# Kernel tuning notes

Hardware: AMD Instinct MI355X
Metric: run time of the kernel (lower is better)

## Reference

```python
import jax, jax.numpy as jnp
import numpy as np

N = 50000
E = 800000
IN_C = 128
HID = 128
HID2 = 256
OUT_C = 40


def setup_inputs() -> dict:
    key = jax.random.key(0)
    ks = jax.random.split(key, 12)
    x = jax.random.normal(ks[0], (N, IN_C), dtype=jnp.float32)
    edge_index = jax.random.randint(ks[1], (2, E), 0, N, dtype=jnp.int64)
    def lin(k, fi, fo):
        # torch Linear default init: U(-1/sqrt(fi), 1/sqrt(fi))
        b = 1.0 / np.sqrt(fi)
        k1, k2 = jax.random.split(k)
        W = jax.random.uniform(k1, (fi, fo), minval=-b, maxval=b, dtype=jnp.float32)
        bvec = jax.random.uniform(k2, (fo,), minval=-b, maxval=b, dtype=jnp.float32)
        return W, bvec
    W1, b1 = lin(ks[2], IN_C, HID)
    W2, b2 = lin(ks[3], HID, HID)
    W3, b3 = lin(ks[4], HID, HID2)
    W4, b4 = lin(ks[5], HID2, HID2)
    Wl, bl = lin(ks[6], HID2, OUT_C)
    return {"x": x, "edge_index": edge_index,
            "W1": W1, "b1": b1, "W2": W2, "b2": b2,
            "W3": W3, "b3": b3, "W4": W4, "b4": b4,
            "Wl": Wl, "bl": bl}


def gin_conv(x, src, dst, Wa, ba, Wb, bb):
    # GINConv, eps=0: h_i = MLP(x_i + sum_{j->i} x_j)
    agg = jax.ops.segment_sum(x[src], dst, num_segments=N)  # [N, d]
    h = x + agg
    h = jax.nn.relu(h @ Wa + ba)
    return h @ Wb + bb


def reference(x, edge_index, W1, b1, W2, b2, W3, b3, W4, b4, Wl, bl):
    src, dst = edge_index[0], edge_index[1]
    h = jax.nn.relu(gin_conv(x, src, dst, W1, b1, W2, b2))
    # dropout p=0.5 is identity in eval mode
    h = jax.nn.relu(gin_conv(h, src, dst, W3, b3, W4, b4))
    return h @ Wl + bl
```

## Files before the change

kernel.cpp:

```cpp
#include <hip/hip_runtime.h>
#include <hip/hip_bf16.h>
#include <hip/hip_fp16.h>
#include <stdint.h>

#define N_NODES 50000
#define E_EDGES 800000
#define NBKT 196
#define PBUF 6144

typedef short s16x8 __attribute__((ext_vector_type(8)));
typedef _Float16 f16x8 __attribute__((ext_vector_type(8)));
typedef float f32x4 __attribute__((ext_vector_type(4)));

__device__ __forceinline__ unsigned short f2h_bits(float f) {
    return __half_as_ushort(__float2half(f));
}
__device__ __forceinline__ float h2f(unsigned short u) {
    __half h = *reinterpret_cast<const __half*>(&u);
    return __half2float(h);
}
__device__ __forceinline__ float2 h2f2(unsigned int u) {
    __half2 h = *reinterpret_cast<const __half2*>(&u);
    return __half22float2(h);
}

__global__ __launch_bounds__(256) void khist_conv(
    const int* __restrict__ dst, int* __restrict__ gbcnt,
    const float* __restrict__ x, unsigned short* __restrict__ xh) {
    __shared__ int bcnt[NBKT];
    int t = threadIdx.x;
    for (int i = t; i < NBKT; i += 256) bcnt[i] = 0;
    __syncthreads();
    int gid = blockIdx.x * 256 + t;
    const int STRIDE = 256 * 256;
    const float4* xv = (const float4*)x;
    for (int e = gid; e < E_EDGES; e += STRIDE) {
        atomicAdd(&bcnt[dst[e] >> 8], 1);
        float4 a = xv[(size_t)2 * e];
        float4 b = xv[(size_t)2 * e + 1];
        s16x8 h;
        h[0] = (short)f2h_bits(a.x); h[1] = (short)f2h_bits(a.y);
        h[2] = (short)f2h_bits(a.z); h[3] = (short)f2h_bits(a.w);
        h[4] = (short)f2h_bits(b.x); h[5] = (short)f2h_bits(b.y);
        h[6] = (short)f2h_bits(b.z); h[7] = (short)f2h_bits(b.w);
        *(s16x8*)(xh + (size_t)e * 8) = h;
    }
    __syncthreads();
    for (int i = t; i < NBKT; i += 256) atomicAdd(&gbcnt[i], bcnt[i]);
}

__global__ void scan_bkt(const int* __restrict__ gbcnt, int* __restrict__ bscan,
                         int* __restrict__ gcur) {
    __shared__ int wsum[4];
    int t = threadIdx.x, lane = t & 63, wid = t >> 6;
    int v = (t < NBKT) ? gbcnt[t] : 0;
    int x = v;
#pragma unroll
    for (int off = 1; off < 64; off <<= 1) {
        int tt = __shfl_up(x, off);
        if (lane >= off) x += tt;
    }
    if (lane == 63) wsum[wid] = x;
    __syncthreads();
    if (t == 0) {
        int s = 0;
#pragma unroll
        for (int i = 0; i < 4; i++) { int tmp = wsum[i]; wsum[i] = s; s += tmp; }
    }
    __syncthreads();
    int excl = x - v + wsum[wid];
    if (t <= NBKT) bscan[t] = excl;
    if (t < NBKT) gcur[t] = excl;
}

__global__ __launch_bounds__(256) void bin_pass(
    const int* __restrict__ src, const int* __restrict__ dst,
    int* __restrict__ gcur, unsigned int* __restrict__ pool) {
    __shared__ unsigned int lbuf[NBKT][64];
    __shared__ int lcnt[NBKT];
    __shared__ int lbase[NBKT];
    int tid = threadIdx.x;
    for (int i = tid; i < NBKT; i += 256) lcnt[i] = 0;
    __syncthreads();
    const int EPG = (E_EDGES + gridDim.x - 1) / gridDim.x;
    int e0 = blockIdx.x * EPG;
    int e1 = e0 + EPG; if (e1 > E_EDGES) e1 = E_EDGES;
    for (int wbase = e0; wbase < e1; wbase += 2048) {
        int wend = wbase + 2048; if (wend > e1) wend = e1;
        int d8[8], s8[8], n8 = 0;
        {
            int e = wbase + tid;
#pragma unroll
            for (int k = 0; k < 8; k++, e += 256)
                if (e < wend) { d8[n8] = dst[e]; s8[n8] = src[e]; n8++; }
        }
        for (int k = 0; k < n8; k++) {
            int d = d8[k];
            unsigned int rec = (unsigned int)(s8[k] & 0xFFFF) |
                               ((unsigned int)(d & 255) << 16);
            int b = d >> 8;
            int slot = atomicAdd(&lcnt[b], 1);
            if (slot < 64) lbuf[b][slot] = rec;
            else pool[atomicAdd(&gcur[b], 1)] = rec;
        }
        __syncthreads();
        if (tid < NBKT) {
            int c = lcnt[tid]; if (c > 64) c = 64;
            int lines = c >> 5;
            if (lines) lbase[tid] = atomicAdd(&gcur[tid], lines * 32);
        }
        __syncthreads();
        {
            int wid = tid >> 6, lane = tid & 63;
            for (int b = wid * 49; b < (wid + 1) * 49; b++) {
                int c = lcnt[b]; if (c > 64) c = 64;
                int lines = c >> 5, rem = c & 31;
                for (int l = 0; l < lines; l++)
                    if (lane < 32)
                        pool[lbase[b] + l * 32 + lane] = lbuf[b][l * 32 + lane];
                if (lines && lane < rem) lbuf[b][lane] = lbuf[b][lines * 32 + lane];
                if (lane == 0) lcnt[b] = rem;
            }
        }
        __syncthreads();
    }
    if (tid < NBKT) {
        int c = lcnt[tid]; if (c > 64) c = 64;
        if (c) lbase[tid] = atomicAdd(&gcur[tid], c);
    }
    __syncthreads();
    {
        int wid = tid >> 6, lane = tid & 63;
        for (int b = wid * 49; b < (wid + 1) * 49; b++) {
            int c = lcnt[b]; if (c > 64) c = 64;
            if (lane < c) pool[lbase[b] + lane] = lbuf[b][lane];
        }
    }
}

__global__ __launch_bounds__(256) void build_csr(
    const unsigned int* __restrict__ pool, const int* __restrict__ bscan,
    int* __restrict__ rowptr, unsigned short* __restrict__ perm) {
    __shared__ int ncnt[256];
    __shared__ int ncur[256];
    __shared__ int wsum[4];
    __shared__ unsigned short pbuf[PBUF];
    int b = blockIdx.x, t = threadIdx.x;
    int base = bscan[b], K = bscan[b + 1] - base;
    ncnt[t] = 0;
    __syncthreads();
    for (int i = t; i < K; i += 256)
        atomicAdd(&ncnt[(pool[base + i] >> 16) & 255], 1);
    __syncthreads();
    int lane = t & 63, wid = t >> 6;
    int v = ncnt[t], x = v;
#pragma unroll
    for (int off = 1; off < 64; off <<= 1) {
        int tt = __shfl_up(x, off);
        if (lane >= off) x += tt;
    }
    if (lane == 63) wsum[wid] = x;
    __syncthreads();
    if (t == 0) {
        int s = 0;
#pragma unroll
        for (int i = 0; i < 4; i++) { int tmp = wsum[i]; wsum[i] = s; s += tmp; }
    }
    __syncthreads();
    int excl = x - v + wsum[wid];
    int node = b * 256 + t;
    if (node <= N_NODES) rowptr[node] = base + excl;
    ncur[t] = excl;
    __syncthreads();
    for (int i = t; i < K; i += 256) {
        unsigned int rec = pool[base + i];
        int nl = (rec >> 16) & 255;
        int pos = atomicAdd(&ncur[nl], 1);
        if (pos < PBUF) pbuf[pos] = (unsigned short)rec;
        else perm[base + pos] = (unsigned short)rec;
    }
    __syncthreads();
    int KK = K < PBUF ? K : PBUF;
    for (int i = t; i < KK; i += 256) perm[base + i] = pbuf[i];
}

__global__ __launch_bounds__(256) void gather_agg_h(
    const unsigned short* __restrict__ feat,
    const int* __restrict__ rowptr,
    const unsigned short* __restrict__ perm,
    unsigned short* __restrict__ out) {
    int node = (blockIdx.x * 256 + threadIdx.x) >> 6;
    if (node >= N_NODES) return;
    int lane = threadIdx.x & 63;
    const unsigned int* fv = (const unsigned int*)feat;
    float2 acc = h2f2(fv[(size_t)node * 64 + lane]);
    int beg = rowptr[node], end = rowptr[node + 1];
    for (int base = beg; base < end; base += 64) {
        int cnt = end - base; if (cnt > 64) cnt = 64;
        int pv = (base + lane < end) ? (int)perm[base + lane] : 0;
        int j = 0;
        for (; j + 3 < cnt; j += 4) {
            int s0 = __shfl(pv, j);
            int s1 = __shfl(pv, j + 1);
            int s2 = __shfl(pv, j + 2);
            int s3 = __shfl(pv, j + 3);
            unsigned int u0 = fv[(size_t)s0 * 64 + lane];
            unsigned int u1 = fv[(size_t)s1 * 64 + lane];
            unsigned int u2 = fv[(size_t)s2 * 64 + lane];
            unsigned int u3 = fv[(size_t)s3 * 64 + lane];
            float2 f0 = h2f2(u0), f1 = h2f2(u1), f2 = h2f2(u2), f3 = h2f2(u3);
            acc.x += (f0.x + f1.x) + (f2.x + f3.x);
            acc.y += (f0.y + f1.y) + (f2.y + f3.y);
        }
        for (; j < cnt; j++) {
            int s = __shfl(pv, j);
            float2 f = h2f2(fv[(size_t)s * 64 + lane]);
            acc.x += f.x;
            acc.y += f.y;
        }
    }
    unsigned int o = (unsigned int)f2h_bits(acc.x) | ((unsigned int)f2h_bits(acc.y) << 16);
    ((unsigned int*)out)[(size_t)node * 64 + lane] = o;
}

__device__ __forceinline__ void prep_one(const float* __restrict__ W,
                                         unsigned short* __restrict__ Whi,
                                         unsigned short* __restrict__ Wlo,
                                         int K, int F, int Fpad, int i) {
    int S = K / 32, T = Fpad / 16;
    int total = T * S * 64;
    if (i >= total) return;
    int lane = i & 63;
    int s = (i >> 6) % S;
    int t = (i >> 6) / S;
    int col = t * 16 + (lane & 15);
    int k0 = s * 32 + (lane >> 4) * 8;
    s16x8 vh, vl;
#pragma unroll
    for (int j = 0; j < 8; j++) {
        float w = (col < F) ? W[(size_t)(k0 + j) * F + col] : 0.f;
        unsigned short h = f2h_bits(w);
        float r = (w - h2f(h)) * 1024.0f;
        vh[j] = (short)h;
        vl[j] = (short)f2h_bits(r);
    }
    *(s16x8*)(Whi + (size_t)i * 8) = vh;
    *(s16x8*)(Wlo + (size_t)i * 8) = vl;
}

__global__ void prep_all(const float* W1, const float* W2, const float* W3,
                         const float* W4, const float* Wl,
                         unsigned short* W1h, unsigned short* W1l,
                         unsigned short* W2h, unsigned short* W2l,
                         unsigned short* W3h, unsigned short* W3l,
                         unsigned short* W4h, unsigned short* W4l,
                         unsigned short* Wlh, unsigned short* Wll) {
    int b = blockIdx.x, t = threadIdx.x;
    if (b < 8)       prep_one(W1, W1h, W1l, 128, 128, 128, b * 256 + t);
    else if (b < 16) prep_one(W2, W2h, W2l, 128, 128, 128, (b - 8) * 256 + t);
    else if (b < 32) prep_one(W3, W3h, W3l, 128, 256, 256, (b - 16) * 256 + t);
    else if (b < 64) prep_one(W4, W4h, W4l, 256, 256, 256, (b - 32) * 256 + t);
    else             prep_one(Wl, Wlh, Wll, 256, 40, 64, (b - 64) * 256 + t);
}

template <int K, int F, int FOUT, bool RELU, int RPW, bool HOUT>
__global__ __launch_bounds__(256) void gemm_h(
    const unsigned short* __restrict__ A,
    const unsigned short* __restrict__ Whi,
    const unsigned short* __restrict__ Wlo,
    const float* __restrict__ bias,
    float* __restrict__ out) {
    constexpr int S = K / 32;
    constexpr int T = F / 16;
    constexpr int TL = T / 4;
    int wave = threadIdx.x >> 6;
    int lane = threadIdx.x & 63;
    int row0 = blockIdx.x * (16 * RPW);
    if (row0 >= N_NODES) return;
    int lm = lane & 15;
    int quad = lane >> 4;
    bool rv[RPW];
#pragma unroll
    for (int r = 0; r < RPW; r++) rv[r] = (row0 + r * 16) < N_NODES;

    f16x8 a[RPW][S];
#pragma unroll
    for (int r = 0; r < RPW; r++) {
        int rr = rv[r] ? row0 + r * 16 : row0;
        const unsigned short* ap = A + (size_t)(rr + lm) * K + quad * 8;
#pragma unroll
        for (int s = 0; s < S; s++)
            a[r][s] = *(const f16x8*)(ap + s * 32);
    }

    f32x4 accH[TL][RPW], accL[TL][RPW];
#pragma unroll
    for (int t = 0; t < TL; t++)
#pragma unroll
        for (int r = 0; r < RPW; r++) {
            f32x4 z = {0.f, 0.f, 0.f, 0.f};
            accH[t][r] = z;
            accL[t][r] = z;
        }

#pragma unroll
    for (int s = 0; s < S; s++) {
#pragma unroll
        for (int t = 0; t < TL; t++) {
            int tg = wave * TL + t;
            const size_t fi = (size_t)((tg * S + s) * 64 + lane) * 8;
            const f16x8 bh = *(const f16x8*)(Whi + fi);
            const f16x8 bl = *(const f16x8*)(Wlo + fi);
#pragma unroll
            for (int r = 0; r < RPW; r++) {
                accH[t][r] = __builtin_amdgcn_mfma_f32_16x16x32_f16(a[r][s], bh, accH[t][r], 0, 0, 0);
                accL[t][r] = __builtin_amdgcn_mfma_f32_16x16x32_f16(a[r][s], bl, accL[t][r], 0, 0, 0);
            }
        }
    }

    const float ls = 1.0f / 1024.0f;
#pragma unroll
    for (int r = 0; r < RPW; r++) {
        if (!rv[r]) break;
        int orow = row0 + r * 16 + quad * 4;
#pragma unroll
        for (int t = 0; t < TL; t++) {
            int col = (wave * TL + t) * 16 + lm;
            if (FOUT < F && col >= FOUT) continue;
            float bv = bias[col];
#pragma unroll
            for (int q = 0; q < 4; q++) {
                float vv = fmaf(accL[t][r][q], ls, accH[t][r][q]) + bv;
                if (RELU) vv = fmaxf(vv, 0.f);
                if (HOUT) {
                    ((unsigned short*)out)[(size_t)(orow + q) * FOUT + col] = f2h_bits(vv);
                } else {
                    out[(size_t)(orow + q) * FOUT + col] = vv;
                }
            }
        }
    }
}

extern "C" void kernel_launch(void* const* d_in, const int* in_sizes, int n_in,
                              void* d_out, int out_size, void* d_ws, size_t ws_size,
                              hipStream_t stream) {
    const float* x  = (const float*)d_in[0];
    const int* ei   = (const int*)d_in[1];
    const float* W1 = (const float*)d_in[2];
    const float* b1 = (const float*)d_in[3];
    const float* W2 = (const float*)d_in[4];
    const float* b2 = (const float*)d_in[5];
    const float* W3 = (const float*)d_in[6];
    const float* b3 = (const float*)d_in[7];
    const float* W4 = (const float*)d_in[8];
    const float* b4 = (const float*)d_in[9];
    const float* Wl = (const float*)d_in[10];
    const float* bl = (const float*)d_in[11];
    float* out = (float*)d_out;

    const int* src = ei;
    const int* dst = ei + E_EDGES;

    char* ws = (char*)d_ws;
    size_t off = 0;
    unsigned short* xh  = (unsigned short*)(ws + off); off += (size_t)N_NODES * 128 * 2;
    unsigned short* hFh = (unsigned short*)(ws + off); off += (size_t)N_NODES * 128 * 2;
    unsigned short* h1h = (unsigned short*)(ws + off); off += (size_t)N_NODES * 128 * 2;
    unsigned short* h2h = (unsigned short*)(ws + off); off += (size_t)N_NODES * 256 * 2;
    unsigned short* h2bh= (unsigned short*)(ws + off); off += (size_t)N_NODES * 256 * 2;
    unsigned short* W1h = (unsigned short*)(ws + off); off += 16384 * 2;
    unsigned short* W1l = (unsigned short*)(ws + off); off += 16384 * 2;
    unsigned short* W2h = (unsigned short*)(ws + off); off += 16384 * 2;
    unsigned short* W2l = (unsigned short*)(ws + off); off += 16384 * 2;
    unsigned short* W3h = (unsigned short*)(ws + off); off += 32768 * 2;
    unsigned short* W3l = (unsigned short*)(ws + off); off += 32768 * 2;
    unsigned short* W4h = (unsigned short*)(ws + off); off += 65536 * 2;
    unsigned short* W4l = (unsigned short*)(ws + off); off += 65536 * 2;
    unsigned short* Wlh = (unsigned short*)(ws + off); off += 16384 * 2;
    unsigned short* Wll = (unsigned short*)(ws + off); off += 16384 * 2;
    off = (off + 255) & ~(size_t)255;
    unsigned int* pool = (unsigned int*)(ws + off); off += (size_t)E_EDGES * 4;
    unsigned short* perm = (unsigned short*)(ws + off); off += (size_t)E_EDGES * 2;
    off = (off + 255) & ~(size_t)255;
    int* rowptr = (int*)(ws + off); off += (size_t)(N_NODES + 1) * 4;
    int* gbcnt  = (int*)(ws + off); off += 256 * 4;
    int* bscan  = (int*)(ws + off); off += 256 * 4;
    int* gcur   = (int*)(ws + off); off += 256 * 4;
    (void)ws_size; (void)in_sizes; (void)n_in; (void)out_size;

    (void)hipMemsetAsync(gbcnt, 0, 256 * 4, stream);
    khist_conv<<<256, 256, 0, stream>>>(dst, gbcnt, x, xh);
    scan_bkt<<<1, 256, 0, stream>>>(gbcnt, bscan, gcur);
    bin_pass<<<256, 256, 0, stream>>>(src, dst, gcur, pool);
    build_csr<<<NBKT, 256, 0, stream>>>(pool, bscan, rowptr, perm);

    prep_all<<<72, 256, 0, stream>>>(W1, W2, W3, W4, Wl,
                                     W1h, W1l, W2h, W2l, W3h, W3l,
                                     W4h, W4l, Wlh, Wll);

    const int aggBlocks = (N_NODES * 64 + 255) / 256;
    const int rblk = (N_NODES + 31) / 32;

    gather_agg_h<<<aggBlocks, 256, 0, stream>>>(xh, rowptr, perm, hFh);
    gemm_h<128, 128, 128, true, 2, true><<<rblk, 256, 0, stream>>>(hFh, W1h, W1l, b1, (float*)h1h);
    gemm_h<128, 128, 128, true, 2, true><<<rblk, 256, 0, stream>>>(h1h, W2h, W2l, b2, (float*)xh);

    gather_agg_h<<<aggBlocks, 256, 0, stream>>>(xh, rowptr, perm, hFh);
    gemm_h<128, 256, 256, true, 2, true><<<rblk, 256, 0, stream>>>(hFh, W3h, W3l, b3, (float*)h2h);
    gemm_h<256, 256, 256, true, 2, true><<<rblk, 256, 0, stream>>>(h2h, W4h, W4l, b4, (float*)h2bh);

    gemm_h<256, 64, 40, false, 2, false><<<rblk, 256, 0, stream>>>(h2bh, Wlh, Wll, bl, out);
}
```

Measured before the change: 315.1 us.

## Store fp16 features in column-panel layout and gather per panel

Feature matrices are now stored as 32-column fp16 panels (panel-major, node-minor) instead of row-major, and the gather kernel processes one 64-byte panel slice per node, with four 16-lane groups handling four neighbors at once and a shuffle reduction at the end. The GEMM loads and half-precision stores are adapted to the panel layout. The aim is to shrink each panel's working set so random neighbor gathers hit in cache better, at the cost of four times as many gather blocks, more passes over rowptr/perm, and 64-byte rather than 256-byte gather granularity. Only the 128-wide layers use the gather; the 256-wide GEMM outputs use the same panel indexing.

```diff
diff --git a/kernel.cpp b/kernel.cpp
--- a/kernel.cpp
+++ b/kernel.cpp
@@ -23,6 +23,7 @@
     __half2 h = *reinterpret_cast<const __half2*>(&u);
     return __half22float2(h);
 }
+
 
 __global__ __launch_bounds__(256) void khist_conv(
     const int* __restrict__ dst, int* __restrict__ gbcnt,
@@ -43,7 +44,8 @@
         h[2] = (short)f2h_bits(a.z); h[3] = (short)f2h_bits(a.w);
         h[4] = (short)f2h_bits(b.x); h[5] = (short)f2h_bits(b.y);
         h[6] = (short)f2h_bits(b.z); h[7] = (short)f2h_bits(b.w);
-        *(s16x8*)(xh + (size_t)e * 8) = h;
+        int nodei = e >> 4, col8 = e & 15;
+        *(s16x8*)(xh + ((size_t)(col8 >> 2) * N_NODES + nodei) * 32 + (col8 & 3) * 8) = h;
     }
     __syncthreads();
     for (int i = t; i < NBKT; i += 256) atomicAdd(&gbcnt[i], bcnt[i]);
@@ -184,43 +186,41 @@
     for (int i = t; i < KK; i += 256) perm[base + i] = pbuf[i];
 }
 
-__global__ __launch_bounds__(256) void gather_agg_h(
+__global__ __launch_bounds__(256) void gather_pass(
     const unsigned short* __restrict__ feat,
     const int* __restrict__ rowptr,
     const unsigned short* __restrict__ perm,
     unsigned short* __restrict__ out) {
-    int node = (blockIdx.x * 256 + threadIdx.x) >> 6;
-    if (node >= N_NODES) return;
+    const int BPP = N_NODES / 4;
+    int p = blockIdx.x / BPP;
+    int node = (blockIdx.x % BPP) * 4 + (threadIdx.x >> 6);
     int lane = threadIdx.x & 63;
-    const unsigned int* fv = (const unsigned int*)feat;
-    float2 acc = h2f2(fv[(size_t)node * 64 + lane]);
+    int grp = lane >> 4, c = lane & 15;
+    const unsigned int* pl = (const unsigned int*)feat + (size_t)p * N_NODES * 16;
+    unsigned int* po = (unsigned int*)out + (size_t)p * N_NODES * 16;
+    float2 acc = {0.f, 0.f};
+    if (grp == 0) acc = h2f2(pl[(size_t)node * 16 + c]);
     int beg = rowptr[node], end = rowptr[node + 1];
     for (int base = beg; base < end; base += 64) {
-        int cnt = end - base; if (cnt > 64) cnt = 64;
+        int wlen = end - base; if (wlen > 64) wlen = 64;
         int pv = (base + lane < end) ? (int)perm[base + lane] : 0;
-        int j = 0;
-        for (; j + 3 < cnt; j += 4) {
-            int s0 = __shfl(pv, j);
-            int s1 = __shfl(pv, j + 1);
-            int s2 = __shfl(pv, j + 2);
-            int s3 = __shfl(pv, j + 3);
-            unsigned int u0 = fv[(size_t)s0 * 64 + lane];
-            unsigned int u1 = fv[(size_t)s1 * 64 + lane];
-            unsigned int u2 = fv[(size_t)s2 * 64 + lane];
-            unsigned int u3 = fv[(size_t)s3 * 64 + lane];
-            float2 f0 = h2f2(u0), f1 = h2f2(u1), f2 = h2f2(u2), f3 = h2f2(u3);
-            acc.x += (f0.x + f1.x) + (f2.x + f3.x);
-            acc.y += (f0.y + f1.y) + (f2.y + f3.y);
-        }
-        for (; j < cnt; j++) {
-            int s = __shfl(pv, j);
-            float2 f = h2f2(fv[(size_t)s * 64 + lane]);
-            acc.x += f.x;
-            acc.y += f.y;
-        }
-    }
-    unsigned int o = (unsigned int)f2h_bits(acc.x) | ((unsigned int)f2h_bits(acc.y) << 16);
-    ((unsigned int*)out)[(size_t)node * 64 + lane] = o;
+        for (int j = 0; j < wlen; j += 4) {
+            int nb = j + grp;
+            int s = __shfl(pv, nb);
+            unsigned int u = pl[(size_t)s * 16 + c];
+            float2 f = h2f2(u);
+            if (nb < wlen) { acc.x += f.x; acc.y += f.y; }
+        }
+    }
+    acc.x += __shfl_xor(acc.x, 16);
+    acc.y += __shfl_xor(acc.y, 16);
+    acc.x += __shfl_xor(acc.x, 32);
+    acc.y += __shfl_xor(acc.y, 32);
+    if (grp == 0) {
+        unsigned int o = (unsigned int)f2h_bits(acc.x) |
+                         ((unsigned int)f2h_bits(acc.y) << 16);
+        po[(size_t)node * 16 + c] = o;
+    }
 }
 
 __device__ __forceinline__ void prep_one(const float* __restrict__ W,
@@ -287,10 +287,9 @@
 #pragma unroll
     for (int r = 0; r < RPW; r++) {
         int rr = rv[r] ? row0 + r * 16 : row0;
-        const unsigned short* ap = A + (size_t)(rr + lm) * K + quad * 8;
 #pragma unroll
         for (int s = 0; s < S; s++)
-            a[r][s] = *(const f16x8*)(ap + s * 32);
+            a[r][s] = *(const f16x8*)(A + ((size_t)s * N_NODES + rr + lm) * 32 + quad * 8);
     }
 
     f32x4 accH[TL][RPW], accL[TL][RPW];
@@ -334,7 +333,7 @@
                 float vv = fmaf(accL[t][r][q], ls, accH[t][r][q]) + bv;
                 if (RELU) vv = fmaxf(vv, 0.f);
                 if (HOUT) {
-                    ((unsigned short*)out)[(size_t)(orow + q) * FOUT + col] = f2h_bits(vv);
+                    ((unsigned short*)out)[((size_t)(col >> 5) * N_NODES + (orow + q)) * 32 + (col & 31)] = f2h_bits(vv);
                 } else {
                     out[(size_t)(orow + q) * FOUT + col] = vv;
                 }
@@ -400,14 +399,14 @@
                                      W1h, W1l, W2h, W2l, W3h, W3l,
                                      W4h, W4l, Wlh, Wll);
 
-    const int aggBlocks = (N_NODES * 64 + 255) / 256;
+    const int gBlocks = 4 * (N_NODES / 4);
     const int rblk = (N_NODES + 31) / 32;
 
-    gather_agg_h<<<aggBlocks, 256, 0, stream>>>(xh, rowptr, perm, hFh);
+    gather_pass<<<gBlocks, 256, 0, stream>>>(xh, rowptr, perm, hFh);
     gemm_h<128, 128, 128, true, 2, true><<<rblk, 256, 0, stream>>>(hFh, W1h, W1l, b1, (float*)h1h);
     gemm_h<128, 128, 128, true, 2, true><<<rblk, 256, 0, stream>>>(h1h, W2h, W2l, b2, (float*)xh);
 
-    gather_agg_h<<<aggBlocks, 256, 0, stream>>>(xh, rowptr, perm, hFh);
+    gather_pass<<<gBlocks, 256, 0, stream>>>(xh, rowptr, perm, hFh);
     gemm_h<128, 256, 256, true, 2, true><<<rblk, 256, 0, stream>>>(hFh, W3h, W3l, b3, (float*)h2h);
     gemm_h<256, 256, 256, true, 2, true><<<rblk, 256, 0, stream>>>(h2h, W4h, W4l, b4, (float*)h2bh);
 
```

After: 391.2 us. +24.2%, slower.
